# Performance work log

Measured on AMD Instinct MI355X. Metric: run time of the kernel, lower is better.

Reference implementation:

```python
import jax, jax.numpy as jnp
import numpy as np

HID = 128
EDGE_FEAT = 4
NUM_G = 20
CUTOFF = 10.0
N_NODES = 20000
N_EDGES = 640000


def setup_inputs() -> dict:
    key = jax.random.key(0)
    ks = jax.random.split(key, 20)
    s = 0.02
    in_e = 2 * HID + EDGE_FEAT + NUM_G  # 280
    inp = {
        "h": jax.random.normal(ks[0], (N_NODES, HID), jnp.float32),
        "x": jax.random.normal(ks[1], (N_NODES, 3), jnp.float32),
        "edge_attr": jax.random.normal(ks[2], (N_EDGES, EDGE_FEAT), jnp.float32),
        "edge_index": jax.random.randint(ks[3], (2, N_EDGES), 0, N_NODES, jnp.int32),
        "mask_ligand": jax.random.randint(ks[4], (N_NODES,), 0, 2, jnp.int32),
        # edge_mlp: 2 linear layers, silu after both (act_last=True)
        "W_e1": jax.random.normal(ks[5], (in_e, HID), jnp.float32) * s,
        "b_e1": jnp.zeros((HID,), jnp.float32),
        "W_e2": jax.random.normal(ks[6], (HID, HID), jnp.float32) * s,
        "b_e2": jnp.zeros((HID,), jnp.float32),
        # edge gate: Linear(hidden,1) + sigmoid
        "W_g": jax.random.normal(ks[7], (HID, 1), jnp.float32) * s,
        "b_g": jnp.zeros((1,), jnp.float32),
        # node_mlp: Linear -> silu -> Linear (no act last)
        "W_n1": jax.random.normal(ks[8], (2 * HID, HID), jnp.float32) * s,
        "b_n1": jnp.zeros((HID,), jnp.float32),
        "W_n2": jax.random.normal(ks[9], (HID, HID), jnp.float32) * s,
        "b_n2": jnp.zeros((HID,), jnp.float32),
        # x_mlp: Linear -> silu -> Linear(no bias, tiny init) -> tanh
        "W_x1": jax.random.normal(ks[10], (HID, HID), jnp.float32) * s,
        "b_x1": jnp.zeros((HID,), jnp.float32),
        "W_x2": jax.random.normal(ks[11], (HID, 1), jnp.float32) * 0.001,
    }
    return inp


def reference(h, x, edge_attr, W_e1, b_e1, W_e2, b_e2, W_g, b_g,
              W_n1, b_n1, W_n2, b_n2, W_x1, b_x1, W_x2,
              edge_index, mask_ligand):
    src, dst = edge_index[0], edge_index[1]
    rel = x[dst] - x[src]                                # [E,3]
    d2 = jnp.sum(rel * rel, axis=-1, keepdims=True)     # [E,1]
    r = jnp.sqrt(d2 + 1e-8)
    # Gaussian smearing RBF
    offset = jnp.linspace(0.0, CUTOFF, NUM_G)
    coeff = -0.5 / (offset[1] - offset[0]) ** 2
    d_feat = jnp.exp(coeff * (r - offset) ** 2)          # [E,NUM_G]
    m_in = jnp.concatenate([h[dst], h[src], d_feat, edge_attr], axis=-1)
    m = jax.nn.silu(m_in @ W_e1 + b_e1)
    m = jax.nn.silu(m @ W_e2 + b_e2)
    g = jax.nn.sigmoid(m @ W_g + b_g)                    # [E,1]
    msg = m * g
    agg = jnp.zeros((h.shape[0], HID), msg.dtype).at[dst].add(msg)
    nm = jax.nn.silu(jnp.concatenate([agg, h], axis=-1) @ W_n1 + b_n1)
    h_out = h + (nm @ W_n2 + b_n2)
    coef = jnp.tanh(jax.nn.silu(m @ W_x1 + b_x1) @ W_x2)  # [E,1]
    vec = rel / (r + 1.0) * coef
    dx = jnp.zeros_like(x).at[dst].add(vec.astype(x.dtype))
    x_out = x + dx * mask_ligand.astype(x.dtype)[:, None]
    return (h_out, x_out)
```

## Files before the change

### kernel.cpp

```cpp
#include <hip/hip_runtime.h>
#include <math.h>

#define HID 128
#define NUM_G 20
#define EF 4
#define NN 20000
#define NE 640000
#define KN1 256
#define TS 136

typedef __attribute__((ext_vector_type(8))) short short8;
typedef __attribute__((ext_vector_type(4))) short short4v;
typedef __attribute__((ext_vector_type(4))) float floatx4;

__device__ __forceinline__ float silu_f(float v){
    return v * __builtin_amdgcn_rcpf(1.0f + __expf(-v));
}
__device__ __forceinline__ float sigm_f(float v){
    return __builtin_amdgcn_rcpf(1.0f + __expf(-v));
}
__device__ __forceinline__ float tanh_f(float v){
    return 1.0f - 2.0f * __builtin_amdgcn_rcpf(1.0f + __expf(2.0f * v));
}
__device__ __forceinline__ unsigned short f2bf(float v){
    unsigned int u = __float_as_uint(v);
    u = (u + 0x7fffu + ((u >> 16) & 1u)) >> 16;
    return (unsigned short)u;
}
__device__ __forceinline__ float bf2f(unsigned short u){
    return __uint_as_float(((unsigned int)u) << 16);
}

__global__ __launch_bounds__(320) void prep_w_kernel(
    const float* __restrict__ W_e1, const float* __restrict__ W_e2,
    const float* __restrict__ W_x1, const float* __restrict__ W_n1,
    const float* __restrict__ W_n2,
    unsigned short* __restrict__ WT1d, unsigned short* __restrict__ WT1s,
    unsigned short* __restrict__ WT1r,
    unsigned short* __restrict__ WT_e2, unsigned short* __restrict__ WT_x1,
    unsigned short* __restrict__ WT_n1, unsigned short* __restrict__ WT_n2)
{
    int n = blockIdx.x;
    int t = threadIdx.x;
    if (t < HID) {
        WT1d[n*HID + t] = f2bf(W_e1[t*HID + n]);
        WT1s[n*HID + t] = f2bf(W_e1[(HID+t)*HID + n]);
        WT_e2[n*HID + t] = f2bf(W_e2[t*HID + n]);
        WT_x1[n*HID + t] = f2bf(W_x1[t*HID + n]);
        WT_n2[n*HID + t] = f2bf(W_n2[t*HID + n]);
    }
    if (t < 32) WT1r[n*32 + t] = (t < NUM_G+EF) ? f2bf(W_e1[(256+t)*HID + n]) : (unsigned short)0;
    if (t < KN1) WT_n1[n*KN1 + t] = f2bf(W_n1[t*HID + n]);
}

__global__ __launch_bounds__(256) void hist_kernel(
    const int* __restrict__ edge_index, int* __restrict__ counts)
{
    int e = blockIdx.x * 256 + threadIdx.x;
    atomicAdd(&counts[edge_index[NE + e]], 1);
}

__global__ __launch_bounds__(1024) void scan_kernel(
    const int* __restrict__ counts, int* __restrict__ cursor)
{
    __shared__ int part[1024];
    const int t = threadIdx.x;
    const int CH = (NN + 1023) / 1024;
    int base = t * CH;
    int s = 0;
    for (int i = 0; i < CH; ++i) { int idx = base + i; if (idx < NN) s += counts[idx]; }
    part[t] = s; __syncthreads();
    for (int off = 1; off < 1024; off <<= 1) {
        int v = (t >= off) ? part[t - off] : 0;
        __syncthreads();
        part[t] += v;
        __syncthreads();
    }
    int run = (t == 0) ? 0 : part[t - 1];
    for (int i = 0; i < CH; ++i) {
        int idx = base + i;
        if (idx < NN) { cursor[idx] = run; run += counts[idx]; }
    }
}

__global__ __launch_bounds__(256) void scatter_kernel(
    const int* __restrict__ edge_index, int* __restrict__ cursor,
    int* __restrict__ order)
{
    int e = blockIdx.x * 256 + threadIdx.x;
    int d = edge_index[NE + e];
    int pos = atomicAdd(&cursor[d], 1);
    order[pos] = e;
}

__global__ __launch_bounds__(64, 4) void pd_kernel(
    const float* __restrict__ h, const float* __restrict__ b_e1,
    const unsigned short* __restrict__ WT1d, const unsigned short* __restrict__ WT1s,
    unsigned short* __restrict__ PD, unsigned short* __restrict__ PS)
{
    __shared__ __align__(16) unsigned short T[16*TS];

    const int lane = threadIdx.x;
    const int quad = lane >> 4;
    const int l15  = lane & 15;
    const int n0   = blockIdx.x * 16;
    const int node = n0 + l15;

    short8 ah[4];
    #pragma unroll
    for (int kc = 0; kc < 4; ++kc) {
        const float* p = h + (size_t)node*HID + kc*32 + quad*8;
        float4 f0 = *(const float4*)(p);
        float4 f1 = *(const float4*)(p + 4);
        short8 v;
        v[0]=(short)f2bf(f0.x); v[1]=(short)f2bf(f0.y); v[2]=(short)f2bf(f0.z); v[3]=(short)f2bf(f0.w);
        v[4]=(short)f2bf(f1.x); v[5]=(short)f2bf(f1.y); v[6]=(short)f2bf(f1.z); v[7]=(short)f2bf(f1.w);
        ah[kc] = v;
    }

    floatx4 ad[8], as[8];
    #pragma unroll
    for (int t = 0; t < 8; ++t) { ad[t] = (floatx4){0,0,0,0}; as[t] = (floatx4){0,0,0,0}; }
    #pragma unroll
    for (int kc = 0; kc < 4; ++kc) {
        #pragma unroll
        for (int t = 0; t < 8; ++t) {
            short8 bd = *(const short8*)(WT1d + (size_t)(t*16+l15)*HID + kc*32 + quad*8);
            short8 bs = *(const short8*)(WT1s + (size_t)(t*16+l15)*HID + kc*32 + quad*8);
            ad[t] = __builtin_amdgcn_mfma_f32_16x16x32_bf16(ah[kc], bd, ad[t], 0, 0, 0);
            as[t] = __builtin_amdgcn_mfma_f32_16x16x32_bf16(ah[kc], bs, as[t], 0, 0, 0);
        }
    }
    #pragma unroll
    for (int t = 0; t < 8; ++t) {
        int col = t*16 + l15;
        float bv = b_e1[col];
        #pragma unroll
        for (int i = 0; i < 4; ++i)
            T[(quad*4+i)*TS + col] = f2bf(ad[t][i] + bv);
    }
    __builtin_amdgcn_wave_barrier();
    #pragma unroll
    for (int kc = 0; kc < 4; ++kc)
        *(short8*)(PD + (size_t)node*HID + kc*32 + quad*8) =
            *(const short8*)(&T[l15*TS + kc*32 + quad*8]);
    __builtin_amdgcn_wave_barrier();
    #pragma unroll
    for (int t = 0; t < 8; ++t) {
        int col = t*16 + l15;
        #pragma unroll
        for (int i = 0; i < 4; ++i)
            T[(quad*4+i)*TS + col] = f2bf(as[t][i]);
    }
    __builtin_amdgcn_wave_barrier();
    #pragma unroll
    for (int kc = 0; kc < 4; ++kc)
        *(short8*)(PS + (size_t)node*HID + kc*32 + quad*8) =
            *(const short8*)(&T[l15*TS + kc*32 + quad*8]);
}

__global__ __launch_bounds__(256, 3) void egnn_edge_mfma(
    const float* __restrict__ x, const float* __restrict__ edge_attr,
    const int* __restrict__ edge_index, const int* __restrict__ order,
    const unsigned short* __restrict__ PD, const unsigned short* __restrict__ PS,
    const unsigned short* __restrict__ WT1r,
    const unsigned short* __restrict__ WT_e2,
    const unsigned short* __restrict__ WT_x1,
    const float* __restrict__ b_e2,
    const float* __restrict__ W_g,  const float* __restrict__ b_g,
    const float* __restrict__ b_x1, const float* __restrict__ W_x2,
    float* __restrict__ agg, float* __restrict__ dxv)
{
    __shared__ __align__(16) unsigned short T[4][32*TS];
    __shared__ int   s_dst[4][33];
    __shared__ float s_g[4][32];
    __shared__ float s_vec[4][96];

    const int wv   = threadIdx.x >> 6;
    const int lane = threadIdx.x & 63;
    const int quad = lane >> 4;
    const int l15  = lane & 15;
    const int e0   = (blockIdx.x * 4 + wv) * 32;

    unsigned short* Tw = &T[wv][0];

    int   ereg = 0, sreg = 0, dreg = 0;
    float rxr = 0.f, ryr = 0.f, rzr = 0.f, rreg = 0.f;
    if (lane < 32) {
        ereg = order[e0 + lane];
        sreg = edge_index[ereg];
        dreg = edge_index[NE + ereg];
        rxr = x[dreg*3+0] - x[sreg*3+0];
        ryr = x[dreg*3+1] - x[sreg*3+1];
        rzr = x[dreg*3+2] - x[sreg*3+2];
        rreg = sqrtf(rxr*rxr + ryr*ryr + rzr*rzr + 1e-8f);
        s_dst[wv][lane] = dreg;
    }
    if (lane == 32) s_dst[wv][32] = -1;

    const int   nd0  = __shfl(dreg, l15);
    const int   ns0  = __shfl(sreg, l15);
    const int   eid0 = __shfl(ereg, l15);
    const float rr0  = __shfl(rreg, l15);
    const int   nd1  = __shfl(dreg, 16 + l15);
    const int   ns1  = __shfl(sreg, 16 + l15);
    const int   eid1 = __shfl(ereg, 16 + l15);
    const float rr1  = __shfl(rreg, 16 + l15);

    short8 pdv0[4], psv0[4], pdv1[4], psv1[4];
    #pragma unroll
    for (int kc = 0; kc < 4; ++kc) {
        pdv0[kc] = *(const short8*)(PD + (size_t)nd0*HID + kc*32 + quad*8);
        psv0[kc] = *(const short8*)(PS + (size_t)ns0*HID + kc*32 + quad*8);
        pdv1[kc] = *(const short8*)(PD + (size_t)nd1*HID + kc*32 + quad*8);
        psv1[kc] = *(const short8*)(PS + (size_t)ns1*HID + kc*32 + quad*8);
    }

    short8 ar0, ar1;
    {
        const float step  = 10.0f / 19.0f;
        const float coeff = -0.5f / (step*step);
        #pragma unroll
        for (int j = 0; j < 8; ++j) {
            int col = quad*8 + j;
            float v0 = 0.f, v1 = 0.f;
            if (col < NUM_G) {
                float d0 = rr0 - step*(float)col;
                float d1 = rr1 - step*(float)col;
                v0 = __expf(coeff*d0*d0);
                v1 = __expf(coeff*d1*d1);
            } else if (col < NUM_G+EF) {
                v0 = edge_attr[(size_t)eid0*EF + (col-NUM_G)];
                v1 = edge_attr[(size_t)eid1*EF + (col-NUM_G)];
            }
            ar0[j] = (short)f2bf(v0);
            ar1[j] = (short)f2bf(v1);
        }
    }

    floatx4 acc0[8], acc1[8];
    #pragma unroll
    for (int t = 0; t < 8; ++t) { acc0[t] = (floatx4){0,0,0,0}; acc1[t] = (floatx4){0,0,0,0}; }
    #pragma unroll
    for (int t = 0; t < 8; ++t) {
        short8 b = *(const short8*)(WT1r + (size_t)(t*16+l15)*32 + quad*8);
        acc0[t] = __builtin_amdgcn_mfma_f32_16x16x32_bf16(ar0, b, acc0[t], 0, 0, 0);
        acc1[t] = __builtin_amdgcn_mfma_f32_16x16x32_bf16(ar1, b, acc1[t], 0, 0, 0);
    }
    #pragma unroll
    for (int t = 0; t < 8; ++t) {
        int col = t*16 + l15;
        #pragma unroll
        for (int i = 0; i < 4; ++i) {
            Tw[(quad*4+i)*TS + col]    = f2bf(acc0[t][i]);
            Tw[(16+quad*4+i)*TS + col] = f2bf(acc1[t][i]);
        }
    }
    __builtin_amdgcn_wave_barrier();

    short8 a2[8];
    #pragma unroll
    for (int kc = 0; kc < 4; ++kc) {
        short8 rv0 = *(const short8*)(&Tw[l15*TS + kc*32 + quad*8]);
        short8 rv1 = *(const short8*)(&Tw[(16+l15)*TS + kc*32 + quad*8]);
        short8 o0, o1;
        #pragma unroll
        for (int j = 0; j < 8; ++j) {
            float v0 = bf2f((unsigned short)pdv0[kc][j])
                     + bf2f((unsigned short)psv0[kc][j])
                     + bf2f((unsigned short)rv0[j]);
            float v1 = bf2f((unsigned short)pdv1[kc][j])
                     + bf2f((unsigned short)psv1[kc][j])
                     + bf2f((unsigned short)rv1[j]);
            o0[j] = (short)f2bf(silu_f(v0));
            o1[j] = (short)f2bf(silu_f(v1));
        }
        a2[kc]   = o0;
        a2[4+kc] = o1;
    }
    __builtin_amdgcn_wave_barrier();

    #pragma unroll
    for (int t = 0; t < 8; ++t) { acc0[t] = (floatx4){0,0,0,0}; acc1[t] = (floatx4){0,0,0,0}; }
    #pragma unroll
    for (int kc = 0; kc < 4; ++kc) {
        #pragma unroll
        for (int t = 0; t < 8; ++t) {
            short8 b = *(const short8*)(WT_e2 + (size_t)(t*16+l15)*HID + kc*32 + quad*8);
            acc0[t] = __builtin_amdgcn_mfma_f32_16x16x32_bf16(a2[kc],   b, acc0[t], 0, 0, 0);
            acc1[t] = __builtin_amdgcn_mfma_f32_16x16x32_bf16(a2[4+kc], b, acc1[t], 0, 0, 0);
        }
    }
    {
        float gp0[4] = {0,0,0,0}, gp1[4] = {0,0,0,0};
        #pragma unroll
        for (int t = 0; t < 8; ++t) {
            int col = t*16 + l15;
            float bv = b_e2[col];
            float wgv = W_g[col];
            #pragma unroll
            for (int i = 0; i < 4; ++i) {
                float m20 = silu_f(acc0[t][i] + bv);
                float m21 = silu_f(acc1[t][i] + bv);
                gp0[i] += m20 * wgv;
                gp1[i] += m21 * wgv;
                Tw[(quad*4+i)*TS + col]    = f2bf(m20);
                Tw[(16+quad*4+i)*TS + col] = f2bf(m21);
            }
        }
        const float bg0 = b_g[0];
        #pragma unroll
        for (int i = 0; i < 4; ++i) {
            gp0[i] += __shfl_xor(gp0[i], 1); gp0[i] += __shfl_xor(gp0[i], 2);
            gp0[i] += __shfl_xor(gp0[i], 4); gp0[i] += __shfl_xor(gp0[i], 8);
            gp1[i] += __shfl_xor(gp1[i], 1); gp1[i] += __shfl_xor(gp1[i], 2);
            gp1[i] += __shfl_xor(gp1[i], 4); gp1[i] += __shfl_xor(gp1[i], 8);
        }
        if (l15 == 0) {
            #pragma unroll
            for (int i = 0; i < 4; ++i) {
                s_g[wv][quad*4 + i]      = sigm_f(gp0[i] + bg0);
                s_g[wv][16 + quad*4 + i] = sigm_f(gp1[i] + bg0);
            }
        }
    }
    __builtin_amdgcn_wave_barrier();

    #pragma unroll
    for (int kc = 0; kc < 4; ++kc) {
        a2[kc]   = *(const short8*)(&Tw[l15*TS + kc*32 + quad*8]);
        a2[4+kc] = *(const short8*)(&Tw[(16+l15)*TS + kc*32 + quad*8]);
    }
    #pragma unroll
    for (int t = 0; t < 8; ++t) { acc0[t] = (floatx4){0,0,0,0}; acc1[t] = (floatx4){0,0,0,0}; }
    #pragma unroll
    for (int kc = 0; kc < 4; ++kc) {
        #pragma unroll
        for (int t = 0; t < 8; ++t) {
            short8 b = *(const short8*)(WT_x1 + (size_t)(t*16+l15)*HID + kc*32 + quad*8);
            acc0[t] = __builtin_amdgcn_mfma_f32_16x16x32_bf16(a2[kc],   b, acc0[t], 0, 0, 0);
            acc1[t] = __builtin_amdgcn_mfma_f32_16x16x32_bf16(a2[4+kc], b, acc1[t], 0, 0, 0);
        }
    }
    {
        float cp0[4] = {0,0,0,0}, cp1[4] = {0,0,0,0};
        #pragma unroll
        for (int t = 0; t < 8; ++t) {
            int col = t*16 + l15;
            float bv = b_x1[col];
            float wx = W_x2[col];
            #pragma unroll
            for (int i = 0; i < 4; ++i) {
                cp0[i] += silu_f(acc0[t][i] + bv) * wx;
                cp1[i] += silu_f(acc1[t][i] + bv) * wx;
            }
        }
        #pragma unroll
        for (int i = 0; i < 4; ++i) {
            cp0[i] += __shfl_xor(cp0[i], 1); cp0[i] += __shfl_xor(cp0[i], 2);
            cp0[i] += __shfl_xor(cp0[i], 4); cp0[i] += __shfl_xor(cp0[i], 8);
            cp1[i] += __shfl_xor(cp1[i], 1); cp1[i] += __shfl_xor(cp1[i], 2);
            cp1[i] += __shfl_xor(cp1[i], 4); cp1[i] += __shfl_xor(cp1[i], 8);
        }
        if (l15 < 3) {
            #pragma unroll
            for (int i = 0; i < 4; ++i) {
                int r0 = quad*4 + i;
                int r1 = 16 + quad*4 + i;
                float relc0 = (l15 == 0) ? __shfl(rxr, r0) : ((l15 == 1) ? __shfl(ryr, r0) : __shfl(rzr, r0));
                float relc1 = (l15 == 0) ? __shfl(rxr, r1) : ((l15 == 1) ? __shfl(ryr, r1) : __shfl(rzr, r1));
                float rv0 = __shfl(rreg, r0);
                float rv1 = __shfl(rreg, r1);
                s_vec[wv][r0*3 + l15] = relc0 * __builtin_amdgcn_rcpf(rv0 + 1.0f) * tanh_f(cp0[i]);
                s_vec[wv][r1*3 + l15] = relc1 * __builtin_amdgcn_rcpf(rv1 + 1.0f) * tanh_f(cp1[i]);
            }
        }
    }
    __builtin_amdgcn_wave_barrier();

    {
        float am0 = 0.f, am1 = 0.f;
        #pragma unroll
        for (int r = 0; r < 32; ++r) {
            unsigned int pv = *(const unsigned int*)(&Tw[r*TS + lane*2]);
            float gr = s_g[wv][r];
            am0 += bf2f((unsigned short)(pv & 0xffffu)) * gr;
            am1 += bf2f((unsigned short)(pv >> 16)) * gr;
            int dr = s_dst[wv][r];
            if (dr != s_dst[wv][r+1]) {
                atomicAdd(&agg[(size_t)dr*HID + lane*2],     am0);
                atomicAdd(&agg[(size_t)dr*HID + lane*2 + 1], am1);
                am0 = 0.f; am1 = 0.f;
            }
        }
    }
    if (lane < 3) {
        float a = 0.f;
        #pragma unroll
        for (int r = 0; r < 32; ++r) {
            a += s_vec[wv][r*3 + lane];
            int dr = s_dst[wv][r];
            if (dr != s_dst[wv][r+1]) {
                atomicAdd(&dxv[(size_t)dr*3 + lane], a);
                a = 0.f;
            }
        }
    }
}

__global__ __launch_bounds__(64, 4) void egnn_node_mfma(
    const float* __restrict__ h, const float* __restrict__ x,
    const int* __restrict__ mask,
    const float* __restrict__ agg, const float* __restrict__ dxv,
    const unsigned short* __restrict__ WT_n1, const float* __restrict__ b_n1,
    const unsigned short* __restrict__ WT_n2, const float* __restrict__ b_n2,
    float* __restrict__ h_out, float* __restrict__ x_out)
{
    __shared__ __align__(16) unsigned short T[16*TS];

    const int lane = threadIdx.x;
    const int quad = lane >> 4;
    const int l15  = lane & 15;
    const int n0   = blockIdx.x * 16;

    if (lane < 48) {
        int r = lane / 3, c = lane % 3;
        int n = n0 + r;
        x_out[n*3 + c] = x[n*3 + c] + dxv[n*3 + c] * (float)mask[n];
    }

    const int node = n0 + l15;
    short8 a1[8];
    #pragma unroll
    for (int kc = 0; kc < 4; ++kc) {
        const float* p = agg + (size_t)node*HID + kc*32 + quad*8;
        float4 f0 = *(const float4*)(p);
        float4 f1 = *(const float4*)(p + 4);
        short8 v;
        v[0]=(short)f2bf(f0.x); v[1]=(short)f2bf(f0.y); v[2]=(short)f2bf(f0.z); v[3]=(short)f2bf(f0.w);
        v[4]=(short)f2bf(f1.x); v[5]=(short)f2bf(f1.y); v[6]=(short)f2bf(f1.z); v[7]=(short)f2bf(f1.w);
        a1[kc] = v;
    }
    #pragma unroll
    for (int kc = 0; kc < 4; ++kc) {
        const float* p = h + (size_t)node*HID + kc*32 + quad*8;
        float4 f0 = *(const float4*)(p);
        float4 f1 = *(const float4*)(p + 4);
        short8 v;
        v[0]=(short)f2bf(f0.x); v[1]=(short)f2bf(f0.y); v[2]=(short)f2bf(f0.z); v[3]=(short)f2bf(f0.w);
        v[4]=(short)f2bf(f1.x); v[5]=(short)f2bf(f1.y); v[6]=(short)f2bf(f1.z); v[7]=(short)f2bf(f1.w);
        a1[4+kc] = v;
    }

    floatx4 acc[8];
    #pragma unroll
    for (int t = 0; t < 8; ++t) acc[t] = (floatx4){0,0,0,0};
    #pragma unroll
    for (int kc = 0; kc < 8; ++kc) {
        #pragma unroll
        for (int t = 0; t < 8; ++t) {
            short8 b = *(const short8*)(WT_n1 + (size_t)(t*16+l15)*KN1 + kc*32 + quad*8);
            acc[t] = __builtin_amdgcn_mfma_f32_16x16x32_bf16(a1[kc], b, acc[t], 0, 0, 0);
        }
    }
    #pragma unroll
    for (int t = 0; t < 8; ++t) {
        int col = t*16 + l15;
        float bv = b_n1[col];
        #pragma unroll
        for (int i = 0; i < 4; ++i)
            T[(quad*4+i)*TS + col] = f2bf(silu_f(acc[t][i] + bv));
    }
    __builtin_amdgcn_wave_barrier();

    short8 a2[4];
    #pragma unroll
    for (int kc = 0; kc < 4; ++kc)
        a2[kc] = *(const short8*)(&T[l15*TS + kc*32 + quad*8]);
    #pragma unroll
    for (int t = 0; t < 8; ++t) acc[t] = (floatx4){0,0,0,0};
    #pragma unroll
    for (int kc = 0; kc < 4; ++kc) {
        #pragma unroll
        for (int t = 0; t < 8; ++t) {
            short8 b = *(const short8*)(WT_n2 + (size_t)(t*16+l15)*HID + kc*32 + quad*8);
            acc[t] = __builtin_amdgcn_mfma_f32_16x16x32_bf16(a2[kc], b, acc[t], 0, 0, 0);
        }
    }
    #pragma unroll
    for (int t = 0; t < 8; ++t) {
        int col = t*16 + l15;
        float bv = b_n2[col];
        #pragma unroll
        for (int i = 0; i < 4; ++i) {
            int n = n0 + quad*4 + i;
            h_out[(size_t)n*HID + col] = h[(size_t)n*HID + col] + acc[t][i] + bv;
        }
    }
}

extern "C" void kernel_launch(void* const* d_in, const int* in_sizes, int n_in,
                              void* d_out, int out_size, void* d_ws, size_t ws_size,
                              hipStream_t stream) {
    const float* h          = (const float*)d_in[0];
    const float* x          = (const float*)d_in[1];
    const float* edge_attr  = (const float*)d_in[2];
    const int*   edge_index = (const int*)  d_in[3];
    const int*   mask       = (const int*)  d_in[4];
    const float* W_e1 = (const float*)d_in[5];
    const float* b_e1 = (const float*)d_in[6];
    const float* W_e2 = (const float*)d_in[7];
    const float* b_e2 = (const float*)d_in[8];
    const float* W_g  = (const float*)d_in[9];
    const float* b_g  = (const float*)d_in[10];
    const float* W_n1 = (const float*)d_in[11];
    const float* b_n1 = (const float*)d_in[12];
    const float* W_n2 = (const float*)d_in[13];
    const float* b_n2 = (const float*)d_in[14];
    const float* W_x1 = (const float*)d_in[15];
    const float* b_x1 = (const float*)d_in[16];
    const float* W_x2 = (const float*)d_in[17];

    char* ws = (char*)d_ws;
    float* agg = (float*)ws;                       ws += (size_t)NN*HID*4;
    float* dxv = (float*)ws;                       ws += (size_t)NN*3*4;
    int*   counts = (int*)ws;                      ws += (size_t)NN*4;
    int*   cursor = (int*)ws;                      ws += (size_t)NN*4;
    int*   order  = (int*)ws;                      ws += (size_t)NE*4;
    unsigned short* PD    = (unsigned short*)ws;   ws += (size_t)NN*HID*2;
    unsigned short* PS    = (unsigned short*)ws;   ws += (size_t)NN*HID*2;
    unsigned short* WT1d  = (unsigned short*)ws;   ws += (size_t)HID*HID*2;
    unsigned short* WT1s  = (unsigned short*)ws;   ws += (size_t)HID*HID*2;
    unsigned short* WT1r  = (unsigned short*)ws;   ws += (size_t)HID*32*2;
    unsigned short* WT_e2 = (unsigned short*)ws;   ws += (size_t)HID*HID*2;
    unsigned short* WT_x1 = (unsigned short*)ws;   ws += (size_t)HID*HID*2;
    unsigned short* WT_n1 = (unsigned short*)ws;   ws += (size_t)HID*KN1*2;
    unsigned short* WT_n2 = (unsigned short*)ws;   ws += (size_t)HID*HID*2;

    hipMemsetAsync(agg, 0, ((size_t)NN*HID + (size_t)NN*3)*sizeof(float), stream);
    hipMemsetAsync(counts, 0, (size_t)NN*sizeof(int), stream);

    prep_w_kernel<<<128, 320, 0, stream>>>(W_e1, W_e2, W_x1, W_n1, W_n2,
                                           WT1d, WT1s, WT1r, WT_e2, WT_x1, WT_n1, WT_n2);
    pd_kernel<<<NN/16, 64, 0, stream>>>(h, b_e1, WT1d, WT1s, PD, PS);
    hist_kernel<<<NE/256, 256, 0, stream>>>(edge_index, counts);
    scan_kernel<<<1, 1024, 0, stream>>>(counts, cursor);
    scatter_kernel<<<NE/256, 256, 0, stream>>>(edge_index, cursor, order);

    egnn_edge_mfma<<<NE/128, 256, 0, stream>>>(
        x, edge_attr, edge_index, order, PD, PS, WT1r, WT_e2, WT_x1,
        b_e2, W_g, b_g, b_x1, W_x2, agg, dxv);

    float* h_out = (float*)d_out;
    float* x_out = h_out + (size_t)NN*HID;

    egnn_node_mfma<<<NN/16, 64, 0, stream>>>(
        h, x, mask, agg, dxv, WT_n1, b_n1, WT_n2, b_n2, h_out, x_out);
}
```

Before: 524.0 us.

## Presort edge data into dst order, fuse prep+hist, pack bf16 conversions

The scatter pass now writes src/dst pairs, the relative position vector, the distance and bf16 edge attributes directly in destination-sorted order. This replaces the indirect order→edge_index→x gathers in the edge kernel with coalesced loads. Weight prep and the histogram are merged into one launch. Scalar bf16 rounding is replaced by packed two-wide intrinsics across all kernels, and the edge kernel block shrinks to 2 waves. The sorted buffers add extra global writes and workspace, and edge attributes are now quantized to bf16 earlier.

Result: slower. 564.2 us (+7.7%).

```diff
diff --git a/kernel.cpp b/kernel.cpp
--- a/kernel.cpp
+++ b/kernel.cpp
@@ -1,4 +1,5 @@
 #include <hip/hip_runtime.h>
+#include <hip/hip_bf16.h>
 #include <math.h>
 
 #define HID 128
@@ -12,6 +13,7 @@
 typedef __attribute__((ext_vector_type(8))) short short8;
 typedef __attribute__((ext_vector_type(4))) short short4v;
 typedef __attribute__((ext_vector_type(4))) float floatx4;
+typedef __attribute__((ext_vector_type(4))) unsigned int uintx4;
 
 __device__ __forceinline__ float silu_f(float v){
     return v * __builtin_amdgcn_rcpf(1.0f + __expf(-v));
@@ -30,34 +32,41 @@
 __device__ __forceinline__ float bf2f(unsigned short u){
     return __uint_as_float(((unsigned int)u) << 16);
 }
-
-__global__ __launch_bounds__(320) void prep_w_kernel(
+__device__ __forceinline__ unsigned int pk2(float a, float b){
+    __hip_bfloat162 h = __float22bfloat162_rn(make_float2(a, b));
+    return *(unsigned int*)&h;
+}
+__device__ __forceinline__ float2 up2(unsigned int u){
+    __hip_bfloat162 h = *(__hip_bfloat162*)&u;
+    return __bfloat1622float2(h);
+}
+
+__global__ __launch_bounds__(320) void prep_hist_kernel(
     const float* __restrict__ W_e1, const float* __restrict__ W_e2,
     const float* __restrict__ W_x1, const float* __restrict__ W_n1,
     const float* __restrict__ W_n2,
     unsigned short* __restrict__ WT1d, unsigned short* __restrict__ WT1s,
     unsigned short* __restrict__ WT1r,
     unsigned short* __restrict__ WT_e2, unsigned short* __restrict__ WT_x1,
-    unsigned short* __restrict__ WT_n1, unsigned short* __restrict__ WT_n2)
-{
-    int n = blockIdx.x;
-    int t = threadIdx.x;
-    if (t < HID) {
-        WT1d[n*HID + t] = f2bf(W_e1[t*HID + n]);
-        WT1s[n*HID + t] = f2bf(W_e1[(HID+t)*HID + n]);
-        WT_e2[n*HID + t] = f2bf(W_e2[t*HID + n]);
-        WT_x1[n*HID + t] = f2bf(W_x1[t*HID + n]);
-        WT_n2[n*HID + t] = f2bf(W_n2[t*HID + n]);
-    }
-    if (t < 32) WT1r[n*32 + t] = (t < NUM_G+EF) ? f2bf(W_e1[(256+t)*HID + n]) : (unsigned short)0;
-    if (t < KN1) WT_n1[n*KN1 + t] = f2bf(W_n1[t*HID + n]);
-}
-
-__global__ __launch_bounds__(256) void hist_kernel(
+    unsigned short* __restrict__ WT_n1, unsigned short* __restrict__ WT_n2,
     const int* __restrict__ edge_index, int* __restrict__ counts)
 {
-    int e = blockIdx.x * 256 + threadIdx.x;
-    atomicAdd(&counts[edge_index[NE + e]], 1);
+    int t = threadIdx.x;
+    if (blockIdx.x < 128) {
+        int n = blockIdx.x;
+        if (t < HID) {
+            WT1d[n*HID + t] = f2bf(W_e1[t*HID + n]);
+            WT1s[n*HID + t] = f2bf(W_e1[(HID+t)*HID + n]);
+            WT_e2[n*HID + t] = f2bf(W_e2[t*HID + n]);
+            WT_x1[n*HID + t] = f2bf(W_x1[t*HID + n]);
+            WT_n2[n*HID + t] = f2bf(W_n2[t*HID + n]);
+        }
+        if (t < 32) WT1r[n*32 + t] = (t < NUM_G+EF) ? f2bf(W_e1[(256+t)*HID + n]) : (unsigned short)0;
+        if (t < KN1) WT_n1[n*KN1 + t] = f2bf(W_n1[t*HID + n]);
+    } else {
+        int e = (blockIdx.x - 128) * 320 + t;
+        atomicAdd(&counts[edge_index[NE + e]], 1);
+    }
 }
 
 __global__ __launch_bounds__(1024) void scan_kernel(
@@ -83,14 +92,26 @@
     }
 }
 
-__global__ __launch_bounds__(256) void scatter_kernel(
-    const int* __restrict__ edge_index, int* __restrict__ cursor,
-    int* __restrict__ order)
+__global__ __launch_bounds__(256) void build_kernel(
+    const int* __restrict__ edge_index, const float* __restrict__ x,
+    const float* __restrict__ edge_attr, int* __restrict__ cursor,
+    int2* __restrict__ pair2, float4* __restrict__ geom4,
+    unsigned short* __restrict__ attrb)
 {
     int e = blockIdx.x * 256 + threadIdx.x;
+    int s = edge_index[e];
     int d = edge_index[NE + e];
     int pos = atomicAdd(&cursor[d], 1);
-    order[pos] = e;
+    float rx = x[d*3+0] - x[s*3+0];
+    float ry = x[d*3+1] - x[s*3+1];
+    float rz = x[d*3+2] - x[s*3+2];
+    float r  = sqrtf(rx*rx + ry*ry + rz*rz + 1e-8f);
+    pair2[pos] = make_int2(s, d);
+    geom4[pos] = make_float4(rx, ry, rz, r);
+    short4v a;
+    #pragma unroll
+    for (int j = 0; j < 4; ++j) a[j] = (short)f2bf(edge_attr[(size_t)e*EF + j]);
+    *(short4v*)(attrb + (size_t)pos*4) = a;
 }
 
 __global__ __launch_bounds__(64, 4) void pd_kernel(
@@ -112,10 +133,10 @@
         const float* p = h + (size_t)node*HID + kc*32 + quad*8;
         float4 f0 = *(const float4*)(p);
         float4 f1 = *(const float4*)(p + 4);
-        short8 v;
-        v[0]=(short)f2bf(f0.x); v[1]=(short)f2bf(f0.y); v[2]=(short)f2bf(f0.z); v[3]=(short)f2bf(f0.w);
-        v[4]=(short)f2bf(f1.x); v[5]=(short)f2bf(f1.y); v[6]=(short)f2bf(f1.z); v[7]=(short)f2bf(f1.w);
-        ah[kc] = v;
+        uintx4 u;
+        u[0] = pk2(f0.x, f0.y); u[1] = pk2(f0.z, f0.w);
+        u[2] = pk2(f1.x, f1.y); u[3] = pk2(f1.z, f1.w);
+        ah[kc] = __builtin_bit_cast(short8, u);
     }
 
     floatx4 ad[8], as[8];
@@ -159,9 +180,9 @@
             *(const short8*)(&T[l15*TS + kc*32 + quad*8]);
 }
 
-__global__ __launch_bounds__(256, 3) void egnn_edge_mfma(
-    const float* __restrict__ x, const float* __restrict__ edge_attr,
-    const int* __restrict__ edge_index, const int* __restrict__ order,
+__global__ __launch_bounds__(128, 4) void egnn_edge_mfma(
+    const int2* __restrict__ pair2, const float4* __restrict__ geom4,
+    const unsigned short* __restrict__ attrb,
     const unsigned short* __restrict__ PD, const unsigned short* __restrict__ PS,
     const unsigned short* __restrict__ WT1r,
     const unsigned short* __restrict__ WT_e2,
@@ -171,41 +192,36 @@
     const float* __restrict__ b_x1, const float* __restrict__ W_x2,
     float* __restrict__ agg, float* __restrict__ dxv)
 {
-    __shared__ __align__(16) unsigned short T[4][32*TS];
-    __shared__ int   s_dst[4][33];
-    __shared__ float s_g[4][32];
-    __shared__ float s_vec[4][96];
+    __shared__ __align__(16) unsigned short T[2][32*TS];
+    __shared__ int   s_dst[2][33];
+    __shared__ float s_g[2][32];
+    __shared__ float s_vec[2][96];
 
     const int wv   = threadIdx.x >> 6;
     const int lane = threadIdx.x & 63;
     const int quad = lane >> 4;
     const int l15  = lane & 15;
-    const int e0   = (blockIdx.x * 4 + wv) * 32;
+    const int e0   = (blockIdx.x * 2 + wv) * 32;
 
     unsigned short* Tw = &T[wv][0];
 
-    int   ereg = 0, sreg = 0, dreg = 0;
+    int   sreg = 0, dreg = 0;
     float rxr = 0.f, ryr = 0.f, rzr = 0.f, rreg = 0.f;
     if (lane < 32) {
-        ereg = order[e0 + lane];
-        sreg = edge_index[ereg];
-        dreg = edge_index[NE + ereg];
-        rxr = x[dreg*3+0] - x[sreg*3+0];
-        ryr = x[dreg*3+1] - x[sreg*3+1];
-        rzr = x[dreg*3+2] - x[sreg*3+2];
-        rreg = sqrtf(rxr*rxr + ryr*ryr + rzr*rzr + 1e-8f);
+        int2  p = pair2[e0 + lane];
+        float4 g = geom4[e0 + lane];
+        sreg = p.x; dreg = p.y;
+        rxr = g.x; ryr = g.y; rzr = g.z; rreg = g.w;
         s_dst[wv][lane] = dreg;
     }
     if (lane == 32) s_dst[wv][32] = -1;
 
-    const int   nd0  = __shfl(dreg, l15);
-    const int   ns0  = __shfl(sreg, l15);
-    const int   eid0 = __shfl(ereg, l15);
-    const float rr0  = __shfl(rreg, l15);
-    const int   nd1  = __shfl(dreg, 16 + l15);
-    const int   ns1  = __shfl(sreg, 16 + l15);
-    const int   eid1 = __shfl(ereg, 16 + l15);
-    const float rr1  = __shfl(rreg, 16 + l15);
+    const int   nd0 = __shfl(dreg, l15);
+    const int   ns0 = __shfl(sreg, l15);
+    const float rr0 = __shfl(rreg, l15);
+    const int   nd1 = __shfl(dreg, 16 + l15);
+    const int   ns1 = __shfl(sreg, 16 + l15);
+    const float rr1 = __shfl(rreg, 16 + l15);
 
     short8 pdv0[4], psv0[4], pdv1[4], psv1[4];
     #pragma unroll
@@ -220,22 +236,32 @@
     {
         const float step  = 10.0f / 19.0f;
         const float coeff = -0.5f / (step*step);
-        #pragma unroll
-        for (int j = 0; j < 8; ++j) {
-            int col = quad*8 + j;
-            float v0 = 0.f, v1 = 0.f;
-            if (col < NUM_G) {
-                float d0 = rr0 - step*(float)col;
-                float d1 = rr1 - step*(float)col;
-                v0 = __expf(coeff*d0*d0);
-                v1 = __expf(coeff*d1*d1);
-            } else if (col < NUM_G+EF) {
-                v0 = edge_attr[(size_t)eid0*EF + (col-NUM_G)];
-                v1 = edge_attr[(size_t)eid1*EF + (col-NUM_G)];
+        uintx4 u0, u1;
+        #pragma unroll
+        for (int jp = 0; jp < 4; ++jp) {
+            float v[4];
+            #pragma unroll
+            for (int half = 0; half < 2; ++half) {
+                float rr = half ? rr1 : rr0;
+                int rowbase = e0 + (half ? 16 : 0) + l15;
+                #pragma unroll
+                for (int q = 0; q < 2; ++q) {
+                    int col = quad*8 + jp*2 + q;
+                    float val = 0.f;
+                    if (col < NUM_G) {
+                        float d = rr - step*(float)col;
+                        val = __expf(coeff*d*d);
+                    } else if (col < NUM_G+EF) {
+                        val = bf2f(attrb[(size_t)rowbase*4 + (col-NUM_G)]);
+                    }
+                    v[half*2 + q] = val;
+                }
             }
-            ar0[j] = (short)f2bf(v0);
-            ar1[j] = (short)f2bf(v1);
-        }
+            u0[jp] = pk2(v[0], v[1]);
+            u1[jp] = pk2(v[2], v[3]);
+        }
+        ar0 = __builtin_bit_cast(short8, u0);
+        ar1 = __builtin_bit_cast(short8, u1);
     }
 
     floatx4 acc0[8], acc1[8];
@@ -251,9 +277,13 @@
     for (int t = 0; t < 8; ++t) {
         int col = t*16 + l15;
         #pragma unroll
-        for (int i = 0; i < 4; ++i) {
-            Tw[(quad*4+i)*TS + col]    = f2bf(acc0[t][i]);
-            Tw[(16+quad*4+i)*TS + col] = f2bf(acc1[t][i]);
+        for (int i = 0; i < 4; i += 2) {
+            unsigned int u0 = pk2(acc0[t][i], acc0[t][i+1]);
+            unsigned int u1 = pk2(acc1[t][i], acc1[t][i+1]);
+            Tw[(quad*4+i)*TS + col]        = (unsigned short)u0;
+            Tw[(quad*4+i+1)*TS + col]      = (unsigned short)(u0 >> 16);
+            Tw[(16+quad*4+i)*TS + col]     = (unsigned short)u1;
+            Tw[(16+quad*4+i+1)*TS + col]   = (unsigned short)(u1 >> 16);
         }
     }
     __builtin_amdgcn_wave_barrier();
@@ -261,22 +291,22 @@
     short8 a2[8];
     #pragma unroll
     for (int kc = 0; kc < 4; ++kc) {
-        short8 rv0 = *(const short8*)(&Tw[l15*TS + kc*32 + quad*8]);
-        short8 rv1 = *(const short8*)(&Tw[(16+l15)*TS + kc*32 + quad*8]);
-        short8 o0, o1;
-        #pragma unroll
-        for (int j = 0; j < 8; ++j) {
-            float v0 = bf2f((unsigned short)pdv0[kc][j])
-                     + bf2f((unsigned short)psv0[kc][j])
-                     + bf2f((unsigned short)rv0[j]);
-            float v1 = bf2f((unsigned short)pdv1[kc][j])
-                     + bf2f((unsigned short)psv1[kc][j])
-                     + bf2f((unsigned short)rv1[j]);
-            o0[j] = (short)f2bf(silu_f(v0));
-            o1[j] = (short)f2bf(silu_f(v1));
-        }
-        a2[kc]   = o0;
-        a2[4+kc] = o1;
+        uintx4 rv0 = __builtin_bit_cast(uintx4, *(const short8*)(&Tw[l15*TS + kc*32 + quad*8]));
+        uintx4 rv1 = __builtin_bit_cast(uintx4, *(const short8*)(&Tw[(16+l15)*TS + kc*32 + quad*8]));
+        uintx4 pu0 = __builtin_bit_cast(uintx4, pdv0[kc]);
+        uintx4 su0 = __builtin_bit_cast(uintx4, psv0[kc]);
+        uintx4 pu1 = __builtin_bit_cast(uintx4, pdv1[kc]);
+        uintx4 su1 = __builtin_bit_cast(uintx4, psv1[kc]);
+        uintx4 o0, o1;
+        #pragma unroll
+        for (int w = 0; w < 4; ++w) {
+            float2 p0 = up2(pu0[w]), s0 = up2(su0[w]), r0 = up2(rv0[w]);
+            float2 p1 = up2(pu1[w]), s1 = up2(su1[w]), r1 = up2(rv1[w]);
+            o0[w] = pk2(silu_f(p0.x + s0.x + r0.x), silu_f(p0.y + s0.y + r0.y));
+            o1[w] = pk2(silu_f(p1.x + s1.x + r1.x), silu_f(p1.y + s1.y + r1.y));
+        }
+        a2[kc]   = __builtin_bit_cast(short8, o0);
+        a2[4+kc] = __builtin_bit_cast(short8, o1);
     }
     __builtin_amdgcn_wave_barrier();
 
@@ -299,13 +329,19 @@
             float bv = b_e2[col];
             float wgv = W_g[col];
             #pragma unroll
-            for (int i = 0; i < 4; ++i) {
-                float m20 = silu_f(acc0[t][i] + bv);
-                float m21 = silu_f(acc1[t][i] + bv);
-                gp0[i] += m20 * wgv;
-                gp1[i] += m21 * wgv;
-                Tw[(quad*4+i)*TS + col]    = f2bf(m20);
-                Tw[(16+quad*4+i)*TS + col] = f2bf(m21);
+            for (int i = 0; i < 4; i += 2) {
+                float m20a = silu_f(acc0[t][i]   + bv);
+                float m20b = silu_f(acc0[t][i+1] + bv);
+                float m21a = silu_f(acc1[t][i]   + bv);
+                float m21b = silu_f(acc1[t][i+1] + bv);
+                gp0[i] += m20a * wgv; gp0[i+1] += m20b * wgv;
+                gp1[i] += m21a * wgv; gp1[i+1] += m21b * wgv;
+                unsigned int u0 = pk2(m20a, m20b);
+                unsigned int u1 = pk2(m21a, m21b);
+                Tw[(quad*4+i)*TS + col]      = (unsigned short)u0;
+                Tw[(quad*4+i+1)*TS + col]    = (unsigned short)(u0 >> 16);
+                Tw[(16+quad*4+i)*TS + col]   = (unsigned short)u1;
+                Tw[(16+quad*4+i+1)*TS + col] = (unsigned short)(u1 >> 16);
             }
         }
         const float bg0 = b_g[0];
@@ -384,8 +420,9 @@
         for (int r = 0; r < 32; ++r) {
             unsigned int pv = *(const unsigned int*)(&Tw[r*TS + lane*2]);
             float gr = s_g[wv][r];
-            am0 += bf2f((unsigned short)(pv & 0xffffu)) * gr;
-            am1 += bf2f((unsigned short)(pv >> 16)) * gr;
+            float2 f = up2(pv);
+            am0 += f.x * gr;
+            am1 += f.y * gr;
             int dr = s_dst[wv][r];
             if (dr != s_dst[wv][r+1]) {
                 atomicAdd(&agg[(size_t)dr*HID + lane*2],     am0);
@@ -436,20 +473,20 @@
         const float* p = agg + (size_t)node*HID + kc*32 + quad*8;
         float4 f0 = *(const float4*)(p);
         float4 f1 = *(const float4*)(p + 4);
-        short8 v;
-        v[0]=(short)f2bf(f0.x); v[1]=(short)f2bf(f0.y); v[2]=(short)f2bf(f0.z); v[3]=(short)f2bf(f0.w);
-        v[4]=(short)f2bf(f1.x); v[5]=(short)f2bf(f1.y); v[6]=(short)f2bf(f1.z); v[7]=(short)f2bf(f1.w);
-        a1[kc] = v;
+        uintx4 u;
+        u[0] = pk2(f0.x, f0.y); u[1] = pk2(f0.z, f0.w);
+        u[2] = pk2(f1.x, f1.y); u[3] = pk2(f1.z, f1.w);
+        a1[kc] = __builtin_bit_cast(short8, u);
     }
     #pragma unroll
     for (int kc = 0; kc < 4; ++kc) {
         const float* p = h + (size_t)node*HID + kc*32 + quad*8;
         float4 f0 = *(const float4*)(p);
         float4 f1 = *(const float4*)(p + 4);
-        short8 v;
-        v[0]=(short)f2bf(f0.x); v[1]=(short)f2bf(f0.y); v[2]=(short)f2bf(f0.z); v[3]=(short)f2bf(f0.w);
-        v[4]=(short)f2bf(f1.x); v[5]=(short)f2bf(f1.y); v[6]=(short)f2bf(f1.z); v[7]=(short)f2bf(f1.w);
-        a1[4+kc] = v;
+        uintx4 u;
+        u[0] = pk2(f0.x, f0.y); u[1] = pk2(f0.z, f0.w);
+        u[2] = pk2(f1.x, f1.y); u[3] = pk2(f1.z, f1.w);
+        a1[4+kc] = __builtin_bit_cast(short8, u);
     }
 
     floatx4 acc[8];
@@ -468,8 +505,11 @@
         int col = t*16 + l15;
         float bv = b_n1[col];
         #pragma unroll
-        for (int i = 0; i < 4; ++i)
-            T[(quad*4+i)*TS + col] = f2bf(silu_f(acc[t][i] + bv));
+        for (int i = 0; i < 4; i += 2) {
+            unsigned int u = pk2(silu_f(acc[t][i] + bv), silu_f(acc[t][i+1] + bv));
+            T[(quad*4+i)*TS + col]   = (unsigned short)u;
+            T[(quad*4+i+1)*TS + col] = (unsigned short)(u >> 16);
+        }
     }
     __builtin_amdgcn_wave_barrier();
 
@@ -526,7 +566,9 @@
     float* dxv = (float*)ws;                       ws += (size_t)NN*3*4;
     int*   counts = (int*)ws;                      ws += (size_t)NN*4;
     int*   cursor = (int*)ws;                      ws += (size_t)NN*4;
-    int*   order  = (int*)ws;                      ws += (size_t)NE*4;
+    int2*  pair2  = (int2*)ws;                     ws += (size_t)NE*8;
+    float4* geom4 = (float4*)ws;                   ws += (size_t)NE*16;
+    unsigned short* attrb = (unsigned short*)ws;   ws += (size_t)NE*4*2;
     unsigned short* PD    = (unsigned short*)ws;   ws += (size_t)NN*HID*2;
     unsigned short* PS    = (unsigned short*)ws;   ws += (size_t)NN*HID*2;
     unsigned short* WT1d  = (unsigned short*)ws;   ws += (size_t)HID*HID*2;
@@ -540,15 +582,17 @@
     hipMemsetAsync(agg, 0, ((size_t)NN*HID + (size_t)NN*3)*sizeof(float), stream);
     hipMemsetAsync(counts, 0, (size_t)NN*sizeof(int), stream);
 
-    prep_w_kernel<<<128, 320, 0, stream>>>(W_e1, W_e2, W_x1, W_n1, W_n2,
-                                           WT1d, WT1s, WT1r, WT_e2, WT_x1, WT_n1, WT_n2);
+    prep_hist_kernel<<<128 + NE/320, 320, 0, stream>>>(
+        W_e1, W_e2, W_x1, W_n1, W_n2,
+        WT1d, WT1s, WT1r, WT_e2, WT_x1, WT_n1, WT_n2,
+        edge_index, counts);
+    scan_kernel<<<1, 1024, 0, stream>>>(counts, cursor);
+    build_kernel<<<NE/256, 256, 0, stream>>>(edge_index, x, edge_attr, cursor,
+                                             pair2, geom4, attrb);
     pd_kernel<<<NN/16, 64, 0, stream>>>(h, b_e1, WT1d, WT1s, PD, PS);
-    hist_kernel<<<NE/256, 256, 0, stream>>>(edge_index, counts);
-    scan_kernel<<<1, 1024, 0, stream>>>(counts, cursor);
-    scatter_kernel<<<NE/256, 256, 0, stream>>>(edge_index, cursor, order);
-
-    egnn_edge_mfma<<<NE/128, 256, 0, stream>>>(
-        x, edge_attr, edge_index, order, PD, PS, WT1r, WT_e2, WT_x1,
+
+    egnn_edge_mfma<<<NE/64, 128, 0, stream>>>(
+        pair2, geom4, attrb, PD, PS, WT1r, WT_e2, WT_x1,
         b_e2, W_g, b_g, b_x1, W_x2, agg, dxv);
 
     float* h_out = (float*)d_out;
```
